# Performance work log

Hardware: AMD Instinct MI355X
Metric: run time of the kernel (lower is better)

Reference implementation:

```python
import jax, jax.numpy as jnp
import numpy as np

EPS = 1e-12  # F.normalize default eps


def _l2_normalize(x):
    # F.normalize(x, p=2) normalizes over dim=1 (channels) by default
    n = jnp.sqrt(jnp.sum(x * x, axis=1, keepdims=True))
    return x / jnp.maximum(n, EPS)


def _cost_volume(left, right, num_disp):
    # left, right: (N, C, H, W)
    l = _l2_normalize(left)
    r = _l2_normalize(right)
    # dot[n,h,x,y] = sum_c l[n,c,h,x] * r[n,c,h,y]   -> (N, H, W, W)
    dot = jnp.einsum('nchx,nchy->nhxy', l, r)
    W = left.shape[-1]
    x = jnp.arange(W)                                   # (W,)
    j = jnp.arange(num_disp)                            # (D,)
    # torch.diagonal(offset=-j) + F.pad((j,0)) picks dot[..., x, x-j] with zeros for x<j
    idx = jnp.clip(x[None, :] - j[:, None], 0, W - 1)   # (D, W)
    g = dot[:, :, x[None, :], idx]                      # (N, H, D, W)
    valid = (x[None, :] >= j[:, None])                  # (D, W)
    g = jnp.where(valid[None, None, :, :], g, jnp.zeros((), dtype=g.dtype))
    return jnp.transpose(g, (0, 2, 1, 3))               # (N, D, H, W)


def setup_inputs() -> dict:
    key = jax.random.key(0)
    ks = jax.random.split(key, 6)
    shapes = [(2, 32, 256, 512), (2, 64, 128, 256), (2, 96, 64, 128)]
    inp = {}
    for i, s in enumerate(shapes):
        inp[f'left{i}'] = jax.random.normal(ks[2 * i], s, dtype=jnp.float32)
        inp[f'right{i}'] = jax.random.normal(ks[2 * i + 1], s, dtype=jnp.float32)
    inp['max_disparity'] = 128
    return inp


def reference(left0, right0, left1, right1, left2, right2, max_disparity):
    lefts = [left0, left1, left2]
    rights = [right0, right1, right2]
    md = min(int(max_disparity), lefts[0].shape[-1])
    cost_volumes = []
    for i, (l, r) in enumerate(zip(lefts, rights)):
        cost_volumes.append(_cost_volume(l, r, md // (2 ** i)))
    return tuple(cost_volumes)
```

## Files before the change

### kernel.cpp

```cpp
#include <hip/hip_runtime.h>

typedef __attribute__((ext_vector_type(8))) short bf16x8;
typedef __attribute__((ext_vector_type(4))) float f32x4;
typedef __attribute__((ext_vector_type(4))) _Float16 f16x4;

static __device__ __forceinline__ unsigned short f32_to_bf16(float f) {
    unsigned int x = __float_as_uint(f);
    x += 0x7fffu + ((x >> 16) & 1u);
    return (unsigned short)(x >> 16);
}

static constexpr int SMEM_BYTES = 21504;

template<int C, int H, int W, int D, int TX>
__device__ __forceinline__
void cv_body(const int bx, const float* __restrict__ Lp, const float* __restrict__ Rp,
             float* __restrict__ out, char* smem)
{
    constexpr int NT = 256;
    constexpr int RS = TX + D;
    constexpr int AS = C + 8;
    constexpr int KC = C / 32;
    constexpr int NSTRIP = TX / 16;
    constexpr int WPS = (NT / 64) / NSTRIP;
    constexpr int NTT = D / 16 + 1;
    constexpr int TPW = (NTT + WPS - 1) / WPS;
    constexpr int STAGE_B = (RS + TX) * AS * 2;
    constexpr int OBUF_B  = D * TX * 2;
    constexpr int UNION_B = STAGE_B > OBUF_B ? STAGE_B : OBUF_B;
    static_assert(UNION_B + (RS + TX) * 4 <= SMEM_BYTES, "lds budget");
    static_assert(TX + RS <= NT, "staging: one column per thread");
    static_assert(WPS * 64 * NSTRIP == NT, "wave partition");

    unsigned short* Abf = (unsigned short*)smem;
    unsigned short* Bbf = Abf + RS * AS;
    char*  obuf = smem;
    float* invA = (float*)(smem + UNION_B);
    float* invB = invA + RS;

    const int tid = threadIdx.x;
    constexpr int NXB = W / TX;
    const int xb = bx % NXB;
    const int h  = (bx / NXB) % H;
    const int n  = bx / (NXB * H);
    const int X0 = xb * TX;

    const size_t CH = (size_t)H * W;
    const float* Lb = Lp + ((size_t)n * C * H + h) * W;
    const float* Rb = Rp + ((size_t)n * C * H + h) * W;

    const int col = tid;
    if (col < TX + RS) {
        const float* src; unsigned short* dst; int g; bool zero;
        if (col < TX) { g = X0 + col;            src = Lb; dst = Bbf + col * AS;        zero = false; }
        else          { g = X0 - D + (col - TX); src = Rb; dst = Abf + (col - TX) * AS; zero = g < 0; }
        float ssq = 0.f;
        if (!zero) {
            #pragma unroll
            for (int c0 = 0; c0 < C; c0 += 8) {
                float v[8];
                #pragma unroll
                for (int k = 0; k < 8; ++k) v[k] = src[(size_t)(c0 + k) * CH + g];
                union { unsigned short us[8]; uint4 q; } p;
                #pragma unroll
                for (int k = 0; k < 8; ++k) { ssq += v[k] * v[k]; p.us[k] = f32_to_bf16(v[k]); }
                *(uint4*)&dst[c0] = p.q;
            }
        } else {
            const uint4 z = {0u, 0u, 0u, 0u};
            #pragma unroll
            for (int c0 = 0; c0 < C; c0 += 8) *(uint4*)&dst[c0] = z;
        }
        const float inv = 1.0f / fmaxf(sqrtf(ssq), 1e-12f);
        if (col < TX) invB[col] = inv; else invA[col - TX] = inv;
    }
    __syncthreads();

    const int wave = tid >> 6, lane = tid & 63;
    const int colc = lane & 15, quad = lane >> 4;
    const int strip = wave % NSTRIP;
    const int tslc  = wave / NSTRIP;

    bf16x8 bfr[KC];
    #pragma unroll
    for (int kc = 0; kc < KC; ++kc)
        bfr[kc] = *(const bf16x8*)&Bbf[(strip * 16 + colc) * AS + kc * 32 + quad * 8];

    const int xl = strip * 16 + colc;
    const float sB = invB[xl];

    f32x4 acc[TPW];
    #pragma unroll
    for (int tt = 0; tt < TPW; ++tt) {
        acc[tt] = {0.f, 0.f, 0.f, 0.f};
        const int t = tslc + tt * WPS;
        if (t < NTT) {
            const int yt = strip + t;
            #pragma unroll
            for (int kc = 0; kc < KC; ++kc) {
                const bf16x8 a =
                    *(const bf16x8*)&Abf[(yt * 16 + colc) * AS + kc * 32 + quad * 8];
                acc[tt] = __builtin_amdgcn_mfma_f32_16x16x32_bf16(a, bfr[kc], acc[tt], 0, 0, 0);
            }
        }
    }
    __syncthreads();

    #pragma unroll
    for (int tt = 0; tt < TPW; ++tt) {
        const int t = tslc + tt * WPS;
        if (t < NTT) {
            const int yt = strip + t;
            const int yb = yt * 16 + quad * 4;
            const int jb = D + xl - yb;
            #pragma unroll
            for (int r = 0; r < 4; ++r) {
                const int j = jb - r;
                if (j >= 0 && j < D) {
                    const float val = acc[tt][r] * sB * invA[yb + r];
                    *(_Float16*)(obuf + (((j * TX + xl) * 2) ^ ((j & 7) << 4))) = (_Float16)val;
                }
            }
        }
    }
    __syncthreads();

    constexpr int JV = TX / 4;
    constexpr int NIT = D * TX / 4 / NT;
    float* orow = out + ((size_t)n * D) * CH + (size_t)h * W + X0;
    #pragma unroll
    for (int it = 0; it < NIT; ++it) {
        const int idx = it * NT + tid;
        const int j = idx / JV, xo = idx % JV;
        const f16x4 hv = *(const f16x4*)(obuf + (((j * TX + xo * 4) * 2) ^ ((j & 7) << 4)));
        f32x4 o;
        o.x = (float)hv.x; o.y = (float)hv.y; o.z = (float)hv.z; o.w = (float)hv.w;
        __builtin_nontemporal_store(o, (f32x4*)&orow[(size_t)j * CH + xo * 4]);
    }
}

constexpr int G0 = 2 * 256 * (512 / 64);
constexpr int G1 = 2 * 128 * (256 / 32);
constexpr int G2 = 2 * 64  * (128 / 32);

static __device__ __forceinline__ int xcd_swz(int b, int nwg) {
    return (b & 7) * (nwg >> 3) + (b >> 3);
}

__global__ __launch_bounds__(256, 5)
void fused_cv(const float* __restrict__ l0, const float* __restrict__ r0, float* __restrict__ o0,
              const float* __restrict__ l1, const float* __restrict__ r1, float* __restrict__ o1,
              const float* __restrict__ l2, const float* __restrict__ r2, float* __restrict__ o2)
{
    __shared__ __align__(16) char smem[SMEM_BYTES];
    const int bid = blockIdx.x;
    if (bid < G0)
        cv_body<32, 256, 512, 128, 64>(xcd_swz(bid, G0), l0, r0, o0, smem);
    else if (bid < G0 + G1)
        cv_body<64, 128, 256,  64, 32>(xcd_swz(bid - G0, G1), l1, r1, o1, smem);
    else
        cv_body<96,  64, 128,  32, 32>(xcd_swz(bid - G0 - G1, G2), l2, r2, o2, smem);
}

extern "C" void kernel_launch(void* const* d_in, const int* in_sizes, int n_in,
                              void* d_out, int out_size, void* d_ws, size_t ws_size,
                              hipStream_t stream) {
    (void)in_sizes; (void)n_in; (void)d_ws; (void)ws_size; (void)out_size;
    const float* l0 = (const float*)d_in[0];
    const float* r0 = (const float*)d_in[1];
    const float* l1 = (const float*)d_in[2];
    const float* r1 = (const float*)d_in[3];
    const float* l2 = (const float*)d_in[4];
    const float* r2 = (const float*)d_in[5];

    float* o0 = (float*)d_out;
    float* o1 = o0 + (size_t)2 * 128 * 256 * 512;
    float* o2 = o1 + (size_t)2 * 64 * 128 * 256;

    fused_cv<<<G0 + G1 + G2, 256, 0, stream>>>(l0, r0, o0, l1, r1, o1, l2, r2, o2);
}
```

Baseline: 255.6 us.

## Split channel staging across threads and shrink level-0 x-tile for more blocks

Level 0 now uses a 32-column x-tile instead of 64, doubling its block count. Levels 1 and 2 split each column's channel staging across two threads, combining the partial sums of squares through a small LDS buffer before the inverse norms are computed. The LDS budget is trimmed and the occupancy hint is raised from 5 to 6 blocks. The aim is more parallelism and shorter per-thread staging loops. The cost is more redundant right-image halo loads per output column at level 0 and an extra LDS reduction step.

```diff
diff --git a/kernel.cpp b/kernel.cpp
--- a/kernel.cpp
+++ b/kernel.cpp
@@ -10,9 +10,9 @@
     return (unsigned short)(x >> 16);
 }
 
-static constexpr int SMEM_BYTES = 21504;
-
-template<int C, int H, int W, int D, int TX>
+static constexpr int SMEM_BYTES = 21120;
+
+template<int C, int H, int W, int D, int TX, int TPC>
 __device__ __forceinline__
 void cv_body(const int bx, const float* __restrict__ Lp, const float* __restrict__ Rp,
              float* __restrict__ out, char* smem)
@@ -25,18 +25,22 @@
     constexpr int WPS = (NT / 64) / NSTRIP;
     constexpr int NTT = D / 16 + 1;
     constexpr int TPW = (NTT + WPS - 1) / WPS;
-    constexpr int STAGE_B = (RS + TX) * AS * 2;
+    constexpr int COLS = TX + RS;
+    constexpr int CPT = C / TPC;
+    constexpr int STAGE_B = COLS * AS * 2;
     constexpr int OBUF_B  = D * TX * 2;
     constexpr int UNION_B = STAGE_B > OBUF_B ? STAGE_B : OBUF_B;
-    static_assert(UNION_B + (RS + TX) * 4 <= SMEM_BYTES, "lds budget");
-    static_assert(TX + RS <= NT, "staging: one column per thread");
-    static_assert(WPS * 64 * NSTRIP == NT, "wave partition");
+    static_assert(UNION_B + COLS * 4 + TPC * COLS * 4 <= SMEM_BYTES, "lds budget");
+    static_assert(COLS * TPC <= NT, "staging partition");
+    static_assert(WPS * NSTRIP * 64 == NT, "wave partition");
+    static_assert(C % (8 * TPC) == 0, "channel split granularity");
 
     unsigned short* Abf = (unsigned short*)smem;
     unsigned short* Bbf = Abf + RS * AS;
     char*  obuf = smem;
     float* invA = (float*)(smem + UNION_B);
     float* invB = invA + RS;
+    float* psum = invB + TX;
 
     const int tid = threadIdx.x;
     constexpr int NXB = W / TX;
@@ -49,15 +53,19 @@
     const float* Lb = Lp + ((size_t)n * C * H + h) * W;
     const float* Rb = Rp + ((size_t)n * C * H + h) * W;
 
-    const int col = tid;
-    if (col < TX + RS) {
-        const float* src; unsigned short* dst; int g; bool zero;
-        if (col < TX) { g = X0 + col;            src = Lb; dst = Bbf + col * AS;        zero = false; }
-        else          { g = X0 - D + (col - TX); src = Rb; dst = Abf + (col - TX) * AS; zero = g < 0; }
+    if (tid < COLS * TPC) {
+        const int sub = tid / COLS;
+        const int col = tid % COLS;
+        const float* src; unsigned short* dst; int g;
+        if (col < TX) { g = X0 + col;            src = Lb; dst = Bbf + col * AS; }
+        else          { g = X0 - D + (col - TX); src = Rb; dst = Abf + (col - TX) * AS; }
+        const bool zero = (col >= TX) && (g < 0);
+        const int c0b = sub * CPT;
         float ssq = 0.f;
         if (!zero) {
             #pragma unroll
-            for (int c0 = 0; c0 < C; c0 += 8) {
+            for (int cc = 0; cc < CPT; cc += 8) {
+                const int c0 = c0b + cc;
                 float v[8];
                 #pragma unroll
                 for (int k = 0; k < 8; ++k) v[k] = src[(size_t)(c0 + k) * CH + g];
@@ -69,12 +77,24 @@
         } else {
             const uint4 z = {0u, 0u, 0u, 0u};
             #pragma unroll
-            for (int c0 = 0; c0 < C; c0 += 8) *(uint4*)&dst[c0] = z;
-        }
-        const float inv = 1.0f / fmaxf(sqrtf(ssq), 1e-12f);
-        if (col < TX) invB[col] = inv; else invA[col - TX] = inv;
+            for (int cc = 0; cc < CPT; cc += 8) *(uint4*)&dst[c0b + cc] = z;
+        }
+        if (TPC == 1) {
+            const float inv = 1.0f / fmaxf(sqrtf(ssq), 1e-12f);
+            if (col < TX) invB[col] = inv; else invA[col - TX] = inv;
+        } else {
+            psum[sub * COLS + col] = ssq;
+        }
     }
     __syncthreads();
+
+    if (TPC > 1 && tid < COLS) {
+        float s = 0.f;
+        #pragma unroll
+        for (int u = 0; u < TPC; ++u) s += psum[u * COLS + tid];
+        const float inv = 1.0f / fmaxf(sqrtf(s), 1e-12f);
+        if (tid < TX) invB[tid] = inv; else invA[tid - TX] = inv;
+    }
 
     const int wave = tid >> 6, lane = tid & 63;
     const int colc = lane & 15, quad = lane >> 4;
@@ -87,7 +107,6 @@
         bfr[kc] = *(const bf16x8*)&Bbf[(strip * 16 + colc) * AS + kc * 32 + quad * 8];
 
     const int xl = strip * 16 + colc;
-    const float sB = invB[xl];
 
     f32x4 acc[TPW];
     #pragma unroll
@@ -106,6 +125,7 @@
     }
     __syncthreads();
 
+    const float sB = invB[xl];
     #pragma unroll
     for (int tt = 0; tt < TPW; ++tt) {
         const int t = tslc + tt * WPS;
@@ -139,7 +159,7 @@
     }
 }
 
-constexpr int G0 = 2 * 256 * (512 / 64);
+constexpr int G0 = 2 * 256 * (512 / 32);
 constexpr int G1 = 2 * 128 * (256 / 32);
 constexpr int G2 = 2 * 64  * (128 / 32);
 
@@ -147,7 +167,7 @@
     return (b & 7) * (nwg >> 3) + (b >> 3);
 }
 
-__global__ __launch_bounds__(256, 5)
+__global__ __launch_bounds__(256, 6)
 void fused_cv(const float* __restrict__ l0, const float* __restrict__ r0, float* __restrict__ o0,
               const float* __restrict__ l1, const float* __restrict__ r1, float* __restrict__ o1,
               const float* __restrict__ l2, const float* __restrict__ r2, float* __restrict__ o2)
@@ -155,11 +175,11 @@
     __shared__ __align__(16) char smem[SMEM_BYTES];
     const int bid = blockIdx.x;
     if (bid < G0)
-        cv_body<32, 256, 512, 128, 64>(xcd_swz(bid, G0), l0, r0, o0, smem);
+        cv_body<32, 256, 512, 128, 32, 1>(xcd_swz(bid, G0), l0, r0, o0, smem);
     else if (bid < G0 + G1)
-        cv_body<64, 128, 256,  64, 32>(xcd_swz(bid - G0, G1), l1, r1, o1, smem);
+        cv_body<64, 128, 256,  64, 32, 2>(xcd_swz(bid - G0, G1), l1, r1, o1, smem);
     else
-        cv_body<96,  64, 128,  32, 32>(xcd_swz(bid - G0 - G1, G2), l2, r2, o2, smem);
+        cv_body<96,  64, 128,  32, 32, 2>(xcd_swz(bid - G0 - G1, G2), l2, r2, o2, smem);
 }
 
 extern "C" void kernel_launch(void* const* d_in, const int* in_sizes, int n_in,
```

After: 258.8 us. About the same (+1.2%).
